# Performance work log

Measured on AMD Instinct MI355X. Metric: run time of the kernel, lower is better.

Reference implementation:

```python
import jax, jax.numpy as jnp
import numpy as np

LRELU = 0.01
EPS = 1e-5
HEADS = 4


def _ln(x, g, b):
    m = x.mean(-1, keepdims=True)
    v = ((x - m) ** 2).mean(-1, keepdims=True)
    return (x - m) / jnp.sqrt(v + EPS) * g + b


def _mapx(x, w1, b1, g1, be1, w2, b2, g2, be2, w3, b3):
    h = jax.nn.leaky_relu(_ln(x @ w1 + b1, g1, be1), LRELU)
    h = jax.nn.leaky_relu(_ln(h @ w2 + b2, g2, be2), LRELU)
    return h @ w3 + b3


def _mcab(x, y, wq, bq, wk, bk, wv, bv, wo, bo, rescale):
    # spectral (channel-wise) multi-head cross attention: q from x, k/v from y
    b, c, h, w = x.shape
    n = h * w
    xt = x.reshape(b, c, n).transpose(0, 2, 1)  # (b, n, c)
    yt = y.reshape(b, c, n).transpose(0, 2, 1)
    dh = c // HEADS
    q = (xt @ wq + bq).reshape(b, n, HEADS, dh).transpose(0, 2, 3, 1)  # (b,H,dh,n)
    k = (yt @ wk + bk).reshape(b, n, HEADS, dh).transpose(0, 2, 3, 1)
    v = (yt @ wv + bv).reshape(b, n, HEADS, dh).transpose(0, 2, 3, 1)
    q = q / (jnp.linalg.norm(q, axis=-1, keepdims=True) + 1e-8)
    k = k / (jnp.linalg.norm(k, axis=-1, keepdims=True) + 1e-8)
    attn = jax.nn.softmax(jnp.einsum('bhdn,bhen->bhde', q, k) * rescale, axis=-1)  # (b,H,dh,dh)
    out = jnp.einsum('bhde,bhen->bhdn', attn, v)  # (b,H,dh,n)
    out = out.transpose(0, 3, 1, 2).reshape(b, n, c) @ wo + bo
    out = out + xt  # residual
    return out.transpose(0, 2, 1).reshape(b, c, h, w)


def setup_inputs() -> dict:
    key = jax.random.key(0)
    ks = jax.random.split(key, 16)
    B, C, H, W, K = 4, 64, 128, 128, 21
    s = 0.02
    nrm = lambda k, shape: jax.random.normal(k, shape, jnp.float32) * s
    return {
        'x': jax.random.normal(ks[0], (B, C, H, W), jnp.float32),
        'semantic': jax.random.uniform(ks[1], (B, K, H, W), jnp.float32),
        'wa': nrm(ks[2], (1, C, 4)), 'ba': jnp.zeros((1, 4), jnp.float32),
        'wb': nrm(ks[3], (20, C, 3)), 'bb': jnp.zeros((20, 3), jnp.float32),
        'in_w': nrm(ks[4], (C, C)), 'in_b': jnp.zeros((C,), jnp.float32),
        'mx_w1': nrm(ks[5], (C, 2 * C)), 'mx_b1': jnp.zeros((2 * C,), jnp.float32),
        'mx_g1': jnp.ones((2 * C,), jnp.float32), 'mx_be1': jnp.zeros((2 * C,), jnp.float32),
        'mx_w2': nrm(ks[6], (2 * C, 2 * C)), 'mx_b2': jnp.zeros((2 * C,), jnp.float32),
        'mx_g2': jnp.ones((2 * C,), jnp.float32), 'mx_be2': jnp.zeros((2 * C,), jnp.float32),
        'mx_w3': nrm(ks[7], (2 * C, C)), 'mx_b3': jnp.zeros((C,), jnp.float32),
        'wq': nrm(ks[8], (C, C)), 'bq': jnp.zeros((C,), jnp.float32),
        'wk': nrm(ks[9], (C, C)), 'bk': jnp.zeros((C,), jnp.float32),
        'wv': nrm(ks[10], (C, C)), 'bv': jnp.zeros((C,), jnp.float32),
        'wo': nrm(ks[11], (C, C)), 'bo': jnp.zeros((C,), jnp.float32),
        'rescale': jnp.ones((HEADS, 1, 1), jnp.float32),
    }


def reference(x, semantic, wa, ba, wb, bb, in_w, in_b,
              mx_w1, mx_b1, mx_g1, mx_be1, mx_w2, mx_b2, mx_g2, mx_be2,
              mx_w3, mx_b3, wq, bq, wk, bk, wv, bv, wo, bo, rescale):
    sem = jax.nn.relu(semantic)            # (b,K,h,w)
    xh = x.transpose(0, 2, 3, 1)           # (b,h,w,c)
    # per-class mask-multiply: (b,K,h,w,c)
    masked = xh[:, None] * sem[:, :, :, :, None]
    # class 0 gets the extra channel (64 = 1*4 + 20*3)
    feat_a = jnp.einsum('bkhwc,kcd->bkhwd', masked[:, :1], wa) + ba[None, :, None, None, :]
    feat_b = jnp.einsum('bkhwc,kcd->bkhwd', masked[:, 1:], wb) + bb[None, :, None, None, :]
    b, _, h, w, _ = feat_a.shape
    feat_a = feat_a.reshape(b, h, w, 4)
    feat_b = jnp.moveaxis(feat_b, 1, 3).reshape(b, h, w, 60)  # preserve class order
    all_feat = jnp.concatenate([feat_a, feat_b], axis=-1)     # (b,h,w,64)
    y = (all_feat @ in_w + in_b).transpose(0, 3, 1, 2)        # (b,c,h,w)
    xm = _mapx(xh, mx_w1, mx_b1, mx_g1, mx_be1, mx_w2, mx_b2, mx_g2, mx_be2, mx_w3, mx_b3)
    xm = xm.transpose(0, 3, 1, 2)
    return _mcab(xm, y, wq, bq, wk, bk, wv, bv, wo, bo, rescale)
```

## Files before the change

kernel.cpp:

```cpp
#include <hip/hip_runtime.h>
#include <hip/hip_bf16.h>

#define NPX 16384
typedef __attribute__((ext_vector_type(8))) short short8;
typedef __attribute__((ext_vector_type(8))) _Float16 half8;
typedef __attribute__((ext_vector_type(4))) _Float16 half4;
typedef __attribute__((ext_vector_type(4))) float f32x4;

#define DEV static __device__ __forceinline__

#define WAB   0
#define WINW  4096
#define W1T   8192
#define W2T   16384
#define W3T   32768
#define WQT   40960
#define WKV   45056
#define WTOT  53248

DEV float lrelu(float v) { return v >= 0.f ? v : 0.01f * v; }
DEV short f2h(float f) { _Float16 h = (_Float16)f; return __builtin_bit_cast(short, h); }
DEV float h2f(short s) { return (float)__builtin_bit_cast(_Float16, s); }
DEV f32x4 mfmah(half8 a, half8 b, f32x4 c) {
    return __builtin_amdgcn_mfma_f32_16x16x32_f16(a, b, c, 0, 0, 0);
}

template<int K, int NT, int M>
DEV void gemmM(const short* __restrict__ A, int pitch,
               const short* __restrict__ WT, f32x4 (&acc)[M][NT])
{
    int lane = threadIdx.x & 63;
    int ln = lane & 15, q8 = (lane >> 4) * 8;
    const short* bp = WT + ln * K + q8;
#pragma unroll
    for (int c0 = 0; c0 < K; c0 += 32) {
        half8 a[M];
#pragma unroll
        for (int m = 0; m < M; ++m)
            a[m] = *(const half8*)(A + (size_t)(m * 16 + ln) * pitch + q8 + c0);
#pragma unroll
        for (int t = 0; t < NT; ++t) {
            half8 b = *(const half8*)(bp + (size_t)t * 16 * K + c0);
#pragma unroll
            for (int m = 0; m < M; ++m) acc[m][t] = mfmah(a[m], b, acc[m][t]);
        }
    }
}

template<int NT, int M>
DEV void acc_biasM(f32x4 (&acc)[M][NT], const float* __restrict__ bias)
{
    int ln = threadIdx.x & 15;
#pragma unroll
    for (int t = 0; t < NT; ++t) {
        float bv = bias[t * 16 + ln];
        f32x4 v = {bv, bv, bv, bv};
#pragma unroll
        for (int m = 0; m < M; ++m) acc[m][t] = v;
    }
}

template<int NT, int M>
DEV void dstoreM(const f32x4 (&acc)[M][NT], short* sD, int pitch)
{
    int lane = threadIdx.x & 63;
    int ln = lane & 15, r0 = (lane >> 4) * 4;
#pragma unroll
    for (int m = 0; m < M; ++m)
#pragma unroll
        for (int t = 0; t < NT; ++t)
#pragma unroll
            for (int r = 0; r < 4; ++r)
                sD[(m * 16 + r0 + r) * pitch + t * 16 + ln] = f2h(acc[m][t][r]);
}

template<int NT, int M>
DEV void ln_regM(f32x4 (&acc)[M][NT], const float* __restrict__ g, const float* __restrict__ be)
{
    int lane = threadIdx.x & 63, ln = lane & 15;
#pragma unroll
    for (int m = 0; m < M; ++m) {
        f32x4 s = {0,0,0,0}, ss = {0,0,0,0};
#pragma unroll
        for (int t = 0; t < NT; ++t)
#pragma unroll
            for (int r = 0; r < 4; ++r) { float v = acc[m][t][r]; s[r] += v; ss[r] += v * v; }
#pragma unroll
        for (int off = 1; off < 16; off <<= 1)
#pragma unroll
            for (int r = 0; r < 4; ++r) {
                s[r] += __shfl_xor(s[r], off);
                ss[r] += __shfl_xor(ss[r], off);
            }
        f32x4 mm, rs;
#pragma unroll
        for (int r = 0; r < 4; ++r) {
            float mean = s[r] * (1.f / 128.f);
            float var = ss[r] * (1.f / 128.f) - mean * mean;
            mm[r] = mean; rs[r] = rsqrtf(var + 1e-5f);
        }
#pragma unroll
        for (int t = 0; t < NT; ++t) {
            float gg = g[t * 16 + ln], bb = be[t * 16 + ln];
#pragma unroll
            for (int r = 0; r < 4; ++r)
                acc[m][t][r] = lrelu((acc[m][t][r] - mm[r]) * rs[r] * gg + bb);
        }
    }
}

template<int ROWS>
DEV void copyoutR(const short* sD, int pitch, short* __restrict__ dst)
{
    int lane = threadIdx.x & 63;
#pragma unroll
    for (int it = 0; it < ROWS / 8; ++it) {
        int idx = it * 512 + lane * 8;
        int px = idx >> 6, c = idx & 63;
        short8 v = *(const short8*)(&sD[px * pitch + c]);
        *reinterpret_cast<short8*>(dst + (size_t)px * 64 + c) = v;
    }
}

DEV void stage_x16(const float* __restrict__ xb, int n0, short* X)
{
    int lane = threadIdx.x & 63;
    int ln = lane & 15, qd = lane >> 4;
    float vb[16];
#pragma unroll
    for (int t = 0; t < 16; ++t)
        vb[t] = xb[(size_t)(qd * 16 + t) * NPX + n0 + ln];
    short8 lo, hi;
#pragma unroll
    for (int t = 0; t < 8; ++t) { lo[t] = f2h(vb[t]); hi[t] = f2h(vb[8 + t]); }
    *reinterpret_cast<short8*>(&X[ln * 72 + qd * 16]) = lo;
    *reinterpret_cast<short8*>(&X[ln * 72 + qd * 16 + 8]) = hi;
}

__global__ __launch_bounds__(256) void k_prep(const float* __restrict__ wa,
                                              const float* __restrict__ wb,
                                              const float* __restrict__ in_w,
                                              const float* __restrict__ w1,
                                              const float* __restrict__ w2,
                                              const float* __restrict__ w3,
                                              const float* __restrict__ wq,
                                              const float* __restrict__ wk,
                                              const float* __restrict__ wv,
                                              short* __restrict__ wt)
{
    int idx = blockIdx.x * 256 + threadIdx.x;
    if (idx >= WTOT) return;
    float v;
    if (idx < WINW) {
        int j = idx >> 6, c = idx & 63;
        v = (j < 4) ? wa[c * 4 + j] : wb[((j - 4) / 3) * 192 + c * 3 + ((j - 4) % 3)];
    } else if (idx < W1T) {
        int i = idx - WINW; v = in_w[(i & 63) * 64 + (i >> 6)];
    } else if (idx < W2T) {
        int i = idx - W1T; v = w1[(i & 63) * 128 + (i >> 6)];
    } else if (idx < W3T) {
        int i = idx - W2T; v = w2[(i & 127) * 128 + (i >> 7)];
    } else if (idx < WQT) {
        int i = idx - W3T; v = w3[(i & 127) * 64 + (i >> 7)];
    } else if (idx < WKV) {
        int i = idx - WQT; v = wq[(i & 63) * 64 + (i >> 6)];
    } else {
        int i = idx - WKV; int e = i >> 6, k = i & 63;
        v = (e < 64) ? wk[k * 64 + e] : wv[k * 64 + (e - 64)];
    }
    wt[idx] = f2h(v);
}

__global__ __launch_bounds__(256, 4) void k_main(const float* __restrict__ x,
                                                 const float* __restrict__ sem,
                                                 const float* __restrict__ ba,
                                                 const float* __restrict__ bbv,
                                                 const float* __restrict__ in_b,
                                                 const float* __restrict__ b1,
                                                 const float* __restrict__ g1,
                                                 const float* __restrict__ be1,
                                                 const float* __restrict__ b2,
                                                 const float* __restrict__ g2,
                                                 const float* __restrict__ be2,
                                                 const float* __restrict__ b3,
                                                 const float* __restrict__ bq,
                                                 const float* __restrict__ bk,
                                                 const float* __restrict__ bv,
                                                 const short* __restrict__ wt,
                                                 short* __restrict__ vout,
                                                 short* __restrict__ xmout,
                                                 float* __restrict__ gram,
                                                 float* __restrict__ nsq)
{
    __shared__ short blob[4][4480];
    int tid = threadIdx.x, w = tid >> 6, lane = tid & 63;
    int ln = lane & 15, qd = lane >> 4, r0 = qd * 4;
    int pw = blockIdx.x * 64 + w * 16;
    int b = pw >> 14, n0 = pw & (NPX - 1);
    const float* xb = x + (size_t)b * 64 * NPX;
    short* X  = blob[w];
    short* T  = blob[w] + 1152;
    short* H  = blob[w] + 2304;
    short* QT = H;
    short* KT = H + 1024;

    stage_x16(xb, n0, X);

    f32x4 acc[1][8];
    acc_biasM<8, 1>(acc, b1);
    gemmM<64, 8, 1>(X, 72, wt + W1T, acc);
    ln_regM<8, 1>(acc, g1, be1);
    dstoreM<8, 1>(acc, H, 136);

    acc_biasM<8, 1>(acc, b2);
    gemmM<128, 8, 1>(H, 136, wt + W2T, acc);
    ln_regM<8, 1>(acc, g2, be2);
    dstoreM<8, 1>(acc, H, 136);

    f32x4 a4[1][4];
    acc_biasM<4, 1>(a4, b3);
    gemmM<128, 4, 1>(H, 136, wt + W3T, a4);
    dstoreM<4, 1>(a4, T, 72);
    copyoutR<16>(T, 72, xmout + (size_t)pw * 64);

    acc_biasM<4, 1>(a4, bq);
    gemmM<64, 4, 1>(T, 72, wt + WQT, a4);
#pragma unroll
    for (int t = 0; t < 4; ++t)
#pragma unroll
        for (int r = 0; r < 4; ++r)
            QT[(t * 16 + ln) * 16 + r0 + r] = f2h(a4[0][t][r]);

    f32x4 a1[1][4];
    { f32x4 z = {0,0,0,0};
      for (int t = 0; t < 4; ++t) a1[0][t] = z; }
    gemmM<64, 4, 1>(X, 72, wt + WAB, a1);
#pragma unroll
    for (int t = 0; t < 4; ++t) {
        int j = t * 16 + ln;
        int cls = (j < 4) ? 0 : 1 + (j - 4) / 3;
        float bias = (j < 4) ? ba[j] : bbv[j - 4];
        f32x4 sm4 = *(const f32x4*)(sem + ((size_t)b * 21 + cls) * NPX + n0 + r0);
#pragma unroll
        for (int r = 0; r < 4; ++r)
            T[(r0 + r) * 72 + j] = f2h(fmaxf(sm4[r], 0.f) * a1[0][t][r] + bias);
    }

    acc_biasM<4, 1>(a4, in_b);
    gemmM<64, 4, 1>(T, 72, wt + WINW, a4);
    dstoreM<4, 1>(a4, X, 72);

    f32x4 a3[1][8];
#pragma unroll
    for (int t = 0; t < 8; ++t) {
        float bvv = (t < 4) ? bk[t * 16 + ln] : bv[(t - 4) * 16 + ln];
        f32x4 vv = {bvv, bvv, bvv, bvv};
        a3[0][t] = vv;
    }
    gemmM<64, 8, 1>(X, 72, wt + WKV, a3);
#pragma unroll
    for (int t = 0; t < 8; ++t)
#pragma unroll
        for (int r = 0; r < 4; ++r) {
            short hv = f2h(a3[0][t][r]);
            if (t < 4) KT[(t * 16 + ln) * 16 + r0 + r] = hv;
            else       T[(r0 + r) * 72 + (t - 4) * 16 + ln] = hv;
        }
    copyoutR<16>(T, 72, vout + (size_t)pw * 64);

    float* scr = (float*)blob[w];
#pragma unroll
    for (int h = 0; h < 4; ++h) {
        half4 qa = *(const half4*)(&QT[(h * 16 + ln) * 16 + r0]);
        half4 ka = *(const half4*)(&KT[(h * 16 + ln) * 16 + r0]);
        half8 qa8 = {0, 0, 0, 0, 0, 0, 0, 0};
        half8 ka8 = {0, 0, 0, 0, 0, 0, 0, 0};
#pragma unroll
        for (int r = 0; r < 4; ++r) { qa8[r] = qa[r]; ka8[r] = ka[r]; }
        f32x4 z = {0, 0, 0, 0};
        f32x4 aqk = mfmah(qa8, ka8, z);
        f32x4 aqq = mfmah(qa8, qa8, z);
        f32x4 akk = mfmah(ka8, ka8, z);
#pragma unroll
        for (int r = 0; r < 4; ++r) {
            int d = r0 + r;
            scr[h * 256 + d * 16 + ln] = aqk[r];
            if (ln == d) {
                scr[1024 + h * 16 + d] = aqq[r];
                scr[1088 + h * 16 + d] = akk[r];
            }
        }
    }
    __syncthreads();
#pragma unroll
    for (int i = 0; i < 4; ++i) {
        int idx = i * 256 + tid;
        float s = 0.f;
#pragma unroll
        for (int ww = 0; ww < 4; ++ww) s += ((const float*)blob[ww])[idx];
        atomicAdd(&gram[(size_t)b * 1024 + idx], s);
    }
    if (tid < 128) {
        float s = 0.f;
#pragma unroll
        for (int ww = 0; ww < 4; ++ww) s += ((const float*)blob[ww])[1024 + tid];
        atomicAdd(&nsq[(tid >> 6) * 256 + b * 64 + (tid & 63)], s);
    }
}

__global__ __launch_bounds__(256) void k_attnM(const float* __restrict__ gram,
                                               const float* __restrict__ nsq,
                                               const float* __restrict__ rescale,
                                               const float* __restrict__ wo,
                                               short* __restrict__ MT)
{
    __shared__ float s_at[1024];
    int b = blockIdx.x, tid = threadIdx.x;
    if (tid < 64) {
        int h = tid >> 4, d = tid & 15;
        float nq = sqrtf(nsq[b * 64 + h * 16 + d]) + 1e-8f;
        float rsc = rescale[h];
        float lg[16];
#pragma unroll
        for (int e = 0; e < 16; ++e) {
            float nk = sqrtf(nsq[256 + b * 64 + h * 16 + e]) + 1e-8f;
            lg[e] = rsc * gram[b * 1024 + h * 256 + d * 16 + e] / (nq * nk);
        }
        float m = lg[0];
#pragma unroll
        for (int e = 1; e < 16; ++e) m = fmaxf(m, lg[e]);
        float ssum = 0.f;
#pragma unroll
        for (int e = 0; e < 16; ++e) { lg[e] = expf(lg[e] - m); ssum += lg[e]; }
        float inv = 1.f / ssum;
#pragma unroll
        for (int e = 0; e < 16; ++e) s_at[h * 256 + d * 16 + e] = lg[e] * inv;
    }
    __syncthreads();
    int he = tid >> 2, h = he >> 4, e = he & 15;
    int cc0 = (tid & 3) * 16;
#pragma unroll
    for (int cx = 0; cx < 16; ++cx) {
        int cc = cc0 + cx;
        float s = 0.f;
#pragma unroll
        for (int d = 0; d < 16; ++d)
            s = fmaf(s_at[h * 256 + d * 16 + e], wo[(h * 16 + d) * 64 + cc], s);
        MT[b * 4096 + cc * 64 + he] = f2h(s);
    }
}

__global__ __launch_bounds__(256) void k_out(const short* __restrict__ v,
                                             const short* __restrict__ xm,
                                             const short* __restrict__ MT,
                                             const float* __restrict__ bo,
                                             float* __restrict__ out)
{
    int tid = threadIdx.x, w = tid >> 6, lane = tid & 63;
    int ln = lane & 15, qd = lane >> 4;
    int pw = blockIdx.x * 64 + w * 16;
    int b = pw >> 14, n0 = pw & (NPX - 1);

    f32x4 acc[1][4];
    acc_biasM<4, 1>(acc, bo);
    gemmM<64, 4, 1>(v + (size_t)pw * 64, 64, MT + b * 4096, acc);

#pragma unroll
    for (int t = 0; t < 4; ++t) {
        int c = t * 16 + ln;
        f32x4 o;
#pragma unroll
        for (int r = 0; r < 4; ++r)
            o[r] = acc[0][t][r] + h2f(xm[(size_t)(pw + qd * 4 + r) * 64 + c]);
        *reinterpret_cast<f32x4*>(out + ((size_t)b * 64 + c) * NPX + n0 + qd * 4) = o;
    }
}

extern "C" void kernel_launch(void* const* d_in, const int* in_sizes, int n_in,
                              void* d_out, int out_size, void* d_ws, size_t ws_size,
                              hipStream_t stream)
{
    const float* x    = (const float*)d_in[0];
    const float* sem  = (const float*)d_in[1];
    const float* wa   = (const float*)d_in[2];
    const float* ba   = (const float*)d_in[3];
    const float* wb   = (const float*)d_in[4];
    const float* bbv  = (const float*)d_in[5];
    const float* in_w = (const float*)d_in[6];
    const float* in_b = (const float*)d_in[7];
    const float* w1   = (const float*)d_in[8];
    const float* b1   = (const float*)d_in[9];
    const float* g1   = (const float*)d_in[10];
    const float* be1  = (const float*)d_in[11];
    const float* w2   = (const float*)d_in[12];
    const float* b2   = (const float*)d_in[13];
    const float* g2   = (const float*)d_in[14];
    const float* be2  = (const float*)d_in[15];
    const float* w3   = (const float*)d_in[16];
    const float* b3   = (const float*)d_in[17];
    const float* wq   = (const float*)d_in[18];
    const float* bq   = (const float*)d_in[19];
    const float* wk   = (const float*)d_in[20];
    const float* bk   = (const float*)d_in[21];
    const float* wv   = (const float*)d_in[22];
    const float* bv   = (const float*)d_in[23];
    const float* wo   = (const float*)d_in[24];
    const float* bo   = (const float*)d_in[25];
    const float* rescale = (const float*)d_in[26];

    char* wsb = (char*)d_ws;
    short* wt   = (short*)wsb;
    short* vpx  = (short*)(wsb + (1u << 20));
    short* xmp  = (short*)(wsb + (1u << 20) + (8u << 20));
    float* gram = (float*)(wsb + (1u << 20) + (16u << 20));
    float* nsq  = gram + 4096;
    short* MT   = (short*)(nsq + 512);

    dim3 blk(256);
    k_prep<<<dim3(208), blk, 0, stream>>>(wa, wb, in_w, w1, w2, w3, wq, wk, wv, wt);
    hipMemsetAsync(gram, 0, (4096 + 512) * sizeof(float), stream);
    k_main<<<dim3(1024), blk, 0, stream>>>(x, sem, ba, bbv, in_b,
                                           b1, g1, be1, b2, g2, be2, b3, bq, bk, bv,
                                           wt, vpx, xmp, gram, nsq);
    k_attnM<<<dim3(4), blk, 0, stream>>>(gram, nsq, rescale, wo, MT);
    k_out<<<dim3(1024), blk, 0, stream>>>(vpx, xmp, MT, bo, (float*)d_out);
}
```

Measured before the change: 196.4 us.

## Double-buffer GEMM operand loads, fold gram memset into prep, store V directly

```diff
diff --git a/kernel.cpp b/kernel.cpp
--- a/kernel.cpp
+++ b/kernel.cpp
@@ -17,6 +17,7 @@
 #define WQT   40960
 #define WKV   45056
 #define WTOT  53248
+#define NZERO 4608
 
 DEV float lrelu(float v) { return v >= 0.f ? v : 0.01f * v; }
 DEV short f2h(float f) { _Float16 h = (_Float16)f; return __builtin_bit_cast(short, h); }
@@ -32,18 +33,27 @@
     int lane = threadIdx.x & 63;
     int ln = lane & 15, q8 = (lane >> 4) * 8;
     const short* bp = WT + ln * K + q8;
+    const short* ap = A + (size_t)ln * pitch + q8;
+    half8 a[2][M], bb[2][NT];
+#pragma unroll
+    for (int m = 0; m < M; ++m) a[0][m] = *(const half8*)(ap + m * 16 * pitch);
+#pragma unroll
+    for (int t = 0; t < NT; ++t) bb[0][t] = *(const half8*)(bp + (size_t)t * 16 * K);
 #pragma unroll
     for (int c0 = 0; c0 < K; c0 += 32) {
-        half8 a[M];
-#pragma unroll
-        for (int m = 0; m < M; ++m)
-            a[m] = *(const half8*)(A + (size_t)(m * 16 + ln) * pitch + q8 + c0);
-#pragma unroll
-        for (int t = 0; t < NT; ++t) {
-            half8 b = *(const half8*)(bp + (size_t)t * 16 * K + c0);
-#pragma unroll
-            for (int m = 0; m < M; ++m) acc[m][t] = mfmah(a[m], b, acc[m][t]);
+        const int cur = (c0 >> 5) & 1, nxt = cur ^ 1;
+        if (c0 + 32 < K) {
+#pragma unroll
+            for (int m = 0; m < M; ++m)
+                a[nxt][m] = *(const half8*)(ap + m * 16 * pitch + c0 + 32);
+#pragma unroll
+            for (int t = 0; t < NT; ++t)
+                bb[nxt][t] = *(const half8*)(bp + (size_t)t * 16 * K + c0 + 32);
         }
+#pragma unroll
+        for (int t = 0; t < NT; ++t)
+#pragma unroll
+            for (int m = 0; m < M; ++m) acc[m][t] = mfmah(a[cur][m], bb[cur][t], acc[m][t]);
     }
 }
 
@@ -146,10 +156,15 @@
                                               const float* __restrict__ wq,
                                               const float* __restrict__ wk,
                                               const float* __restrict__ wv,
-                                              short* __restrict__ wt)
+                                              short* __restrict__ wt,
+                                              float* __restrict__ gz)
 {
     int idx = blockIdx.x * 256 + threadIdx.x;
-    if (idx >= WTOT) return;
+    if (idx >= WTOT) {
+        int z = idx - WTOT;
+        if (z < NZERO) gz[z] = 0.f;
+        return;
+    }
     float v;
     if (idx < WINW) {
         int j = idx >> 6, c = idx & 63;
@@ -259,14 +274,15 @@
     }
     gemmM<64, 8, 1>(X, 72, wt + WKV, a3);
 #pragma unroll
-    for (int t = 0; t < 8; ++t)
-#pragma unroll
-        for (int r = 0; r < 4; ++r) {
-            short hv = f2h(a3[0][t][r]);
-            if (t < 4) KT[(t * 16 + ln) * 16 + r0 + r] = hv;
-            else       T[(r0 + r) * 72 + (t - 4) * 16 + ln] = hv;
-        }
-    copyoutR<16>(T, 72, vout + (size_t)pw * 64);
+    for (int t = 0; t < 4; ++t)
+#pragma unroll
+        for (int r = 0; r < 4; ++r)
+            KT[(t * 16 + ln) * 16 + r0 + r] = f2h(a3[0][t][r]);
+#pragma unroll
+    for (int t = 4; t < 8; ++t)
+#pragma unroll
+        for (int r = 0; r < 4; ++r)
+            vout[(size_t)(pw + r0 + r) * 64 + (t - 4) * 16 + ln] = f2h(a3[0][t][r]);
 
     float* scr = (float*)blob[w];
 #pragma unroll
@@ -417,8 +433,7 @@
     short* MT   = (short*)(nsq + 512);
 
     dim3 blk(256);
-    k_prep<<<dim3(208), blk, 0, stream>>>(wa, wb, in_w, w1, w2, w3, wq, wk, wv, wt);
-    hipMemsetAsync(gram, 0, (4096 + 512) * sizeof(float), stream);
+    k_prep<<<dim3(226), blk, 0, stream>>>(wa, wb, in_w, w1, w2, w3, wq, wk, wv, wt, gram);
     k_main<<<dim3(1024), blk, 0, stream>>>(x, sem, ba, bbv, in_b,
                                            b1, g1, be1, b2, g2, be2, b3, bq, bk, bv,
                                            wt, vpx, xmp, gram, nsq);
```

Result: slower. 200.9 us (+2.3%).
